# Optimization experiments

Measured on AMD Instinct MI355X. Metric: run time of the kernel, lower is better.

Reference implementation:

```python
import jax, jax.numpy as jnp
import numpy as np

B, N, X_DIM, Y_DIM, K = 256, 65536, 32, 64, 8
SIGMA_INIT = 0.01

def setup_inputs() -> dict:
    key = jax.random.key(0)
    k1, k2, k3, k4 = jax.random.split(key, 4)
    return {
        "x": jax.random.normal(k1, (B, X_DIM), dtype=jnp.float32),
        "pos_matrix": jax.random.normal(k2, (N, X_DIM), dtype=jnp.float32),
        "project_matrix": jax.random.normal(k3, (N, X_DIM, K), dtype=jnp.float32),
        "color_matrix": jax.random.normal(k4, (N, Y_DIM), dtype=jnp.float32),
        "sigma_matrix": jnp.full((N, K), SIGMA_INIT, dtype=jnp.float32),
    }

def reference(x, pos_matrix, project_matrix, color_matrix, sigma_matrix):
    # x_diff = (x[:,None,:] - pos[None,:,:]) @ P  -> (B, N, k)
    # computed without materializing (B, N, x_dim):
    xP = jnp.einsum('bi,nio->bno', x, project_matrix)          # (B, N, k)
    posP = jnp.einsum('ni,nio->no', pos_matrix, project_matrix)  # (N, k)
    x_diff = xP - posP[None, :, :]                               # (B, N, k)
    # Gaussian kernel per modality
    g = jnp.exp(-x_diff ** 2 / (2.0 * sigma_matrix ** 2))        # (B, N, k)
    # color = g^T @ color_matrix per batch -> (B, k, y_dim)
    color = jnp.einsum('bnk,ny->bky', g, color_matrix)
    return color
```

## Files before the change

kernel.cpp:

```cpp
#include <hip/hip_runtime.h>


typedef __attribute__((ext_vector_type(8))) short short8;
typedef __attribute__((ext_vector_type(4))) float f32x4;

#define NTOT   65536
#define XD     32
#define YD     64
#define KK     8
#define META_BYTES (NTOT*KK*8)
#define PART_FLOATS 32768
#define NCHUNKS 2048

__device__ __forceinline__ unsigned short f2bf(float f) {
  unsigned u = __float_as_uint(f);
  u += 0x7FFFu + ((u >> 16) & 1u);
  return (unsigned short)(u >> 16);
}

__device__ __forceinline__ void gload16(const void* g, void* l) {
  __builtin_amdgcn_global_load_lds(
      (const __attribute__((address_space(1))) unsigned*)g,
      (__attribute__((address_space(3))) unsigned*)l, 16, 0, 0);
}

union FragU { unsigned u[4]; short8 s8; };

__global__ __launch_bounds__(256)
void gaf_pre(const float* __restrict__ pos, const float* __restrict__ proj,
             const float* __restrict__ sig, float2* __restrict__ meta) {
  int gid = blockIdx.x * 256 + threadIdx.x;
  int n = gid >> 3, k = gid & 7;
  const float*  pk = proj + (size_t)n * XD * KK + k;
  const float4* pg = (const float4*)(pos + (size_t)n * XD);
  float d = 0.f;
#pragma unroll
  for (int j = 0; j < 8; ++j) {
    float4 v = pg[j];
    d = fmaf(v.x, pk[(4*j+0)*KK], d);
    d = fmaf(v.y, pk[(4*j+1)*KK], d);
    d = fmaf(v.z, pk[(4*j+2)*KK], d);
    d = fmaf(v.w, pk[(4*j+3)*KK], d);
  }
  float s = sig[gid];
  meta[gid] = make_float2(d, -0.72134752044448169f / (s * s));
}

__global__ __launch_bounds__(512, 4)
void gaf_main(const float* __restrict__ x, const float* __restrict__ proj,
              const float* __restrict__ colr, const float2* __restrict__ meta,
              float* __restrict__ partial, int NCH, int NR) {
  __shared__ unsigned short sPool[2*256*40 + 64*40];
  __shared__ float sPosP[8][36];
  __shared__ float sInv[8][36];
  __shared__ __align__(16) float rawP[32*XD*KK];
  unsigned short (*sPb0)[40] = (unsigned short(*)[40])sPool;
  unsigned short (*sPb1)[40] = (unsigned short(*)[40])(sPool + 256*40);
  unsigned short (*sCol)[40] = (unsigned short(*)[40])(sPool + 2*256*40);

  const int t = threadIdx.x, l = t & 63, w = t >> 6;

  int nr, sblk;
  {
    const int gid = blockIdx.x;
    if ((NR & 7) == 0) {
      const int xcd = gid & 7, j = gid >> 3;
      nr   = xcd * (NR >> 3) + (j >> 2);
      sblk = j & 3;
    } else { nr = gid >> 2; sblk = gid & 3; }
  }

  const int bt = w & 3, k0 = (w >> 2) * 4;
  const int lc = l & 15, lg = l >> 4;
  const int cbeg = nr * NCH;
  int cend = cbeg + NCH; if (cend > NCHUNKS) cend = NCHUNKS;

  float* pb = partial + (size_t)(nr * 4 + sblk) * PART_FLOATS;
  if (cbeg >= cend) {
    float4 z = {0.f,0.f,0.f,0.f};
#pragma unroll
    for (int r = 0; r < PART_FLOATS/4/512; ++r) ((float4*)pb)[t + r*512] = z;
    return;
  }

  short8 xf0, xf1;
  {
    const int brow = sblk*64 + bt*16 + lc;
    const float4* xr = (const float4*)(x + (size_t)brow*XD + lg*8);
    float4 u0 = xr[0], u1 = xr[1];
    float xv[8] = {u0.x,u0.y,u0.z,u0.w,u1.x,u1.y,u1.z,u1.w};
#pragma unroll
    for (int j = 0; j < 8; ++j) {
      unsigned u = __float_as_uint(xv[j]);
      unsigned short h0 = (unsigned short)(u >> 16);
      float r1 = xv[j] - __uint_as_float(u & 0xFFFF0000u);
      xf0[j] = (short)h0;
      xf1[j] = (short)f2bf(r1);
    }
  }

  f32x4 acc[4][4];
#pragma unroll
  for (int a = 0; a < 4; ++a)
#pragma unroll
    for (int b = 0; b < 4; ++b) acc[a][b] = (f32x4){0.f,0.f,0.f,0.f};

  const float4* colr4 = (const float4*)colr;

  auto ISSUE_P = [&](int c) {
    const float4* Pg = (const float4*)(proj + (size_t)c * 32 * XD * KK);
#pragma unroll
    for (int r = 0; r < 4; ++r)
      gload16(Pg + (t + r*512), &rawP[(w*64 + r*512) * 4]);
  };

  ISSUE_P(cbeg);
  for (int c = cbeg; c < cend; ++c) {
    __syncthreads();
    float4 cpf = colr4[(size_t)c * 512 + t];
    float2 mpf;
    if (t < 256) mpf = meta[(size_t)c * 256 + t];
    {
      const float4* raw4 = (const float4*)rawP;
#pragma unroll
      for (int r = 0; r < 2; ++r) {
        const int f0 = ((t >> 1) << 2) + (t & 1) + r * 1024;
        float4 va = raw4[f0], vb = raw4[f0 + 2];
        const int nn = (f0 >> 6) & 31, i0 = (f0 & 63) >> 1, kk4 = (f0 & 1) << 2;
        float ea[4] = {va.x, va.y, va.z, va.w};
        float eb[4] = {vb.x, vb.y, vb.z, vb.w};
#pragma unroll
        for (int jj = 0; jj < 4; ++jj) {
          const int row = (kk4 + jj) * 32 + nn;
          unsigned hi, lo;
          asm("v_cvt_pk_bf16_f32 %0, %1, %2" : "=v"(hi) : "v"(ea[jj]), "v"(eb[jj]));
          float r0 = ea[jj] - __uint_as_float(hi << 16);
          float r1 = eb[jj] - __uint_as_float(hi & 0xFFFF0000u);
          asm("v_cvt_pk_bf16_f32 %0, %1, %2" : "=v"(lo) : "v"(r0), "v"(r1));
          *(unsigned*)&sPb0[row][i0] = hi;
          *(unsigned*)&sPb1[row][i0] = lo;
        }
      }
    }
    {
      int n = t >> 4, y4 = (t & 15) * 4;
      sCol[y4+0][n] = f2bf(cpf.x);
      sCol[y4+1][n] = f2bf(cpf.y);
      sCol[y4+2][n] = f2bf(cpf.z);
      sCol[y4+3][n] = f2bf(cpf.w);
    }
    if (t < 256) { sPosP[t&7][t>>3] = mpf.x; sInv[t&7][t>>3] = mpf.y; }
    __syncthreads();
    if (c + 1 < cend) ISSUE_P(c + 1);

#pragma unroll
    for (int kk = 0; kk < 4; ++kk) {
      const int k = k0 + kk;
      FragU gb;
      {
        const int prow = k*32 + lc;
        short8 p0 = *(const short8*)&sPb0[prow][lg*8];
        short8 p1 = *(const short8*)&sPb1[prow][lg*8];
        f32x4 S = (f32x4){0.f,0.f,0.f,0.f};
        S = __builtin_amdgcn_mfma_f32_16x16x32_bf16(p1, xf1, S, 0, 0, 0);
        S = __builtin_amdgcn_mfma_f32_16x16x32_bf16(p1, xf0, S, 0, 0, 0);
        S = __builtin_amdgcn_mfma_f32_16x16x32_bf16(p0, xf1, S, 0, 0, 0);
        S = __builtin_amdgcn_mfma_f32_16x16x32_bf16(p0, xf0, S, 0, 0, 0);
        float4 pp = *(const float4*)&sPosP[k][lg*4];
        float4 iv = *(const float4*)&sInv[k][lg*4];
        float d0 = S[0]-pp.x, d1 = S[1]-pp.y, d2 = S[2]-pp.z, d3 = S[3]-pp.w;
        float g0 = __builtin_amdgcn_exp2f(d0*d0*iv.x);
        float g1 = __builtin_amdgcn_exp2f(d1*d1*iv.y);
        float g2 = __builtin_amdgcn_exp2f(d2*d2*iv.z);
        float g3 = __builtin_amdgcn_exp2f(d3*d3*iv.w);
        asm("v_cvt_pk_bf16_f32 %0, %1, %2" : "=v"(gb.u[0]) : "v"(g0), "v"(g1));
        asm("v_cvt_pk_bf16_f32 %0, %1, %2" : "=v"(gb.u[1]) : "v"(g2), "v"(g3));
      }
      {
        const int prow = k*32 + 16 + lc;
        short8 p0 = *(const short8*)&sPb0[prow][lg*8];
        short8 p1 = *(const short8*)&sPb1[prow][lg*8];
        f32x4 S = (f32x4){0.f,0.f,0.f,0.f};
        S = __builtin_amdgcn_mfma_f32_16x16x32_bf16(p1, xf1, S, 0, 0, 0);
        S = __builtin_amdgcn_mfma_f32_16x16x32_bf16(p1, xf0, S, 0, 0, 0);
        S = __builtin_amdgcn_mfma_f32_16x16x32_bf16(p0, xf1, S, 0, 0, 0);
        S = __builtin_amdgcn_mfma_f32_16x16x32_bf16(p0, xf0, S, 0, 0, 0);
        float4 pp = *(const float4*)&sPosP[k][16 + lg*4];
        float4 iv = *(const float4*)&sInv[k][16 + lg*4];
        float d0 = S[0]-pp.x, d1 = S[1]-pp.y, d2 = S[2]-pp.z, d3 = S[3]-pp.w;
        float g0 = __builtin_amdgcn_exp2f(d0*d0*iv.x);
        float g1 = __builtin_amdgcn_exp2f(d1*d1*iv.y);
        float g2 = __builtin_amdgcn_exp2f(d2*d2*iv.z);
        float g3 = __builtin_amdgcn_exp2f(d3*d3*iv.w);
        asm("v_cvt_pk_bf16_f32 %0, %1, %2" : "=v"(gb.u[2]) : "v"(g0), "v"(g1));
        asm("v_cvt_pk_bf16_f32 %0, %1, %2" : "=v"(gb.u[3]) : "v"(g2), "v"(g3));
      }
#pragma unroll
      for (int ys = 0; ys < 4; ++ys) {
        FragU af;
        *(uint2*)&af.u[0] = *(const uint2*)&sCol[ys*16 + lc][lg*4];
        *(uint2*)&af.u[2] = *(const uint2*)&sCol[ys*16 + lc][16 + lg*4];
        acc[kk][ys] = __builtin_amdgcn_mfma_f32_16x16x32_bf16(af.s8, gb.s8,
                                                              acc[kk][ys], 0, 0, 0);
      }
    }
  }
  __syncthreads();

  float* epi = (float*)sPool + w * (64*17);
#pragma unroll
  for (int kk = 0; kk < 4; ++kk) {
    const int k = k0 + kk;
#pragma unroll
    for (int ys = 0; ys < 4; ++ys) {
#pragma unroll
      for (int r = 0; r < 4; ++r)
        epi[(ys*16 + lg*4 + r)*17 + lc] = acc[kk][ys][r];
    }
    __syncthreads();
#pragma unroll
    for (int it = 0; it < 4; ++it) {
      int bi = it*4 + lg, y0 = lc*4;
      float4 v = { epi[(y0+0)*17 + bi], epi[(y0+1)*17 + bi],
                   epi[(y0+2)*17 + bi], epi[(y0+3)*17 + bi] };
      *(float4*)&pb[(size_t)(bt*16 + bi)*512 + k*64 + y0] = v;
    }
    __syncthreads();
  }
}

__global__ __launch_bounds__(512)
void gaf_reduce(const float* __restrict__ partial, float* __restrict__ out, int NR) {
  const int b = blockIdx.x;
  const int s = b >> 6, bl = b & 63;
  const int t = threadIdx.x;
  float a0 = 0.f, a1 = 0.f, a2 = 0.f, a3 = 0.f;
  int nr = 0;
  for (; nr + 4 <= NR; nr += 4) {
    a0 += partial[(size_t)((nr+0)*4 + s)*PART_FLOATS + bl*512 + t];
    a1 += partial[(size_t)((nr+1)*4 + s)*PART_FLOATS + bl*512 + t];
    a2 += partial[(size_t)((nr+2)*4 + s)*PART_FLOATS + bl*512 + t];
    a3 += partial[(size_t)((nr+3)*4 + s)*PART_FLOATS + bl*512 + t];
  }
  for (; nr < NR; ++nr)
    a0 += partial[(size_t)(nr*4 + s)*PART_FLOATS + bl*512 + t];
  out[(size_t)b*512 + t] = (a0 + a1) + (a2 + a3);
}

extern "C" void kernel_launch(void* const* d_in, const int* in_sizes, int n_in,
                              void* d_out, int out_size, void* d_ws, size_t ws_size,
                              hipStream_t stream) {
  const float* x    = (const float*)d_in[0];
  const float* pos  = (const float*)d_in[1];
  const float* proj = (const float*)d_in[2];
  const float* colr = (const float*)d_in[3];
  const float* sig  = (const float*)d_in[4];
  float* out = (float*)d_out;

  float2* meta    = (float2*)d_ws;
  float*  partial = (float*)((char*)d_ws + META_BYTES);

  size_t avail = (ws_size > META_BYTES) ? ws_size - META_BYTES : 0;
  int NR = (int)(avail / (4ull * PART_FLOATS * 4ull));
  if (NR > 128) NR = 128;
  if (NR < 1)  NR = 1;
  if (NR >= 8) NR &= ~7;
  int NCH = (NCHUNKS + NR - 1) / NR;

  gaf_pre<<<(NTOT*KK)/256, 256, 0, stream>>>(pos, proj, sig, meta);
  gaf_main<<<4*NR, 512, 0, stream>>>(x, proj, colr, meta, partial, NCH, NR);
  gaf_reduce<<<256, 512, 0, stream>>>(partial, out, NR);
}
```

Baseline: 105.8 us.

## Repack projection tiles into MFMA fragment order with padded staging to cut LDS conflicts

The raw projection staging buffer gets a padded per-row stride (260 floats), and the bf16 hi/lo projection tiles are stored directly in per-lane MFMA fragment order, so each lane reads its operand as one contiguous 16-byte load. The color tile load is reorganized so each thread gathers four n-values for one y and writes them as a packed uint2 using hardware bf16 conversion instead of four scalar software-rounded stores. The aim is fewer LDS bank conflicts and fewer LDS instructions in the per-chunk staging and the MFMA operand fetch. The price is more complex index math and strided global reads of the color matrix.

```diff
diff --git a/kernel.cpp b/kernel.cpp
--- a/kernel.cpp
+++ b/kernel.cpp
@@ -11,12 +11,7 @@
 #define META_BYTES (NTOT*KK*8)
 #define PART_FLOATS 32768
 #define NCHUNKS 2048
-
-__device__ __forceinline__ unsigned short f2bf(float f) {
-  unsigned u = __float_as_uint(f);
-  u += 0x7FFFu + ((u >> 16) & 1u);
-  return (unsigned short)(u >> 16);
-}
+#define CSTR   40
 
 __device__ __forceinline__ void gload16(const void* g, void* l) {
   __builtin_amdgcn_global_load_lds(
@@ -50,13 +45,13 @@
 void gaf_main(const float* __restrict__ x, const float* __restrict__ proj,
               const float* __restrict__ colr, const float2* __restrict__ meta,
               float* __restrict__ partial, int NCH, int NR) {
-  __shared__ unsigned short sPool[2*256*40 + 64*40];
+  __shared__ __align__(16) unsigned short sPool[16*512*2 + 64*CSTR];
   __shared__ float sPosP[8][36];
   __shared__ float sInv[8][36];
-  __shared__ __align__(16) float rawP[32*XD*KK];
-  unsigned short (*sPb0)[40] = (unsigned short(*)[40])sPool;
-  unsigned short (*sPb1)[40] = (unsigned short(*)[40])(sPool + 256*40);
-  unsigned short (*sCol)[40] = (unsigned short(*)[40])(sPool + 2*256*40);
+  __shared__ __align__(16) float rawP[32*260];
+  unsigned short* sPb0 = sPool;
+  unsigned short* sPb1 = sPool + 16*512;
+  unsigned short (*sCol)[CSTR] = (unsigned short(*)[CSTR])(sPool + 2*16*512);
 
   const int t = threadIdx.x, l = t & 63, w = t >> 6;
 
@@ -94,8 +89,10 @@
       unsigned u = __float_as_uint(xv[j]);
       unsigned short h0 = (unsigned short)(u >> 16);
       float r1 = xv[j] - __uint_as_float(u & 0xFFFF0000u);
+      unsigned ur = __float_as_uint(r1);
+      ur += 0x7FFFu + ((ur >> 16) & 1u);
       xf0[j] = (short)h0;
-      xf1[j] = (short)f2bf(r1);
+      xf1[j] = (short)(unsigned short)(ur >> 16);
     }
   }
 
@@ -105,49 +102,59 @@
 #pragma unroll
     for (int b = 0; b < 4; ++b) acc[a][b] = (f32x4){0.f,0.f,0.f,0.f};
 
-  const float4* colr4 = (const float4*)colr;
+  const int kp  = l & 1;
+  const int ipL = (l >> 1) & 3;
+  const int nS  = ((l >> 3) & 7) | ((w & 3) << 3);
+  const int sS  = nS >> 4;
+  const int ldst= (nS & 15);
 
   auto ISSUE_P = [&](int c) {
     const float4* Pg = (const float4*)(proj + (size_t)c * 32 * XD * KK);
 #pragma unroll
-    for (int r = 0; r < 4; ++r)
-      gload16(Pg + (t + r*512), &rawP[(w*64 + r*512) * 4]);
+    for (int r2 = 0; r2 < 4; ++r2) {
+      const int nd = w + r2*8;
+      gload16(Pg + nd*64 + l, &rawP[nd*260]);
+    }
   };
 
   ISSUE_P(cbeg);
   for (int c = cbeg; c < cend; ++c) {
     __syncthreads();
-    float4 cpf = colr4[(size_t)c * 512 + t];
+    const int yq = w*8 + (l>>3);
+    const int nq = (l&7)*4;
+    const float* cb = colr + (size_t)(c*32 + nq)*YD + yq;
+    float c0 = cb[0], c1 = cb[YD], c2 = cb[2*YD], c3 = cb[3*YD];
     float2 mpf;
     if (t < 256) mpf = meta[(size_t)c * 256 + t];
     {
       const float4* raw4 = (const float4*)rawP;
 #pragma unroll
       for (int r = 0; r < 2; ++r) {
-        const int f0 = ((t >> 1) << 2) + (t & 1) + r * 1024;
+        const int ip = ipL | (((w >> 2) & 1) << 2) | (r << 3);
+        const int f0 = nS * 65 + ip * 4 + kp;
         float4 va = raw4[f0], vb = raw4[f0 + 2];
-        const int nn = (f0 >> 6) & 31, i0 = (f0 & 63) >> 1, kk4 = (f0 & 1) << 2;
+        const int l_dst = ldst | ((ip >> 2) << 4);
+        const int wd = ip & 3;
         float ea[4] = {va.x, va.y, va.z, va.w};
         float eb[4] = {vb.x, vb.y, vb.z, vb.w};
 #pragma unroll
         for (int jj = 0; jj < 4; ++jj) {
-          const int row = (kk4 + jj) * 32 + nn;
+          const int ks = (kp*4 + jj)*2 + sS;
           unsigned hi, lo;
           asm("v_cvt_pk_bf16_f32 %0, %1, %2" : "=v"(hi) : "v"(ea[jj]), "v"(eb[jj]));
           float r0 = ea[jj] - __uint_as_float(hi << 16);
           float r1 = eb[jj] - __uint_as_float(hi & 0xFFFF0000u);
           asm("v_cvt_pk_bf16_f32 %0, %1, %2" : "=v"(lo) : "v"(r0), "v"(r1));
-          *(unsigned*)&sPb0[row][i0] = hi;
-          *(unsigned*)&sPb1[row][i0] = lo;
+          ((unsigned*)sPb0)[ks*256 + l_dst*4 + wd] = hi;
+          ((unsigned*)sPb1)[ks*256 + l_dst*4 + wd] = lo;
         }
       }
     }
     {
-      int n = t >> 4, y4 = (t & 15) * 4;
-      sCol[y4+0][n] = f2bf(cpf.x);
-      sCol[y4+1][n] = f2bf(cpf.y);
-      sCol[y4+2][n] = f2bf(cpf.z);
-      sCol[y4+3][n] = f2bf(cpf.w);
+      unsigned w0, w1;
+      asm("v_cvt_pk_bf16_f32 %0, %1, %2" : "=v"(w0) : "v"(c0), "v"(c1));
+      asm("v_cvt_pk_bf16_f32 %0, %1, %2" : "=v"(w1) : "v"(c2), "v"(c3));
+      *(uint2*)&sCol[yq][nq] = make_uint2(w0, w1);
     }
     if (t < 256) { sPosP[t&7][t>>3] = mpf.x; sInv[t&7][t>>3] = mpf.y; }
     __syncthreads();
@@ -158,9 +165,8 @@
       const int k = k0 + kk;
       FragU gb;
       {
-        const int prow = k*32 + lc;
-        short8 p0 = *(const short8*)&sPb0[prow][lg*8];
-        short8 p1 = *(const short8*)&sPb1[prow][lg*8];
+        short8 p0 = *(const short8*)&sPb0[(k*2+0)*512 + l*8];
+        short8 p1 = *(const short8*)&sPb1[(k*2+0)*512 + l*8];
         f32x4 S = (f32x4){0.f,0.f,0.f,0.f};
         S = __builtin_amdgcn_mfma_f32_16x16x32_bf16(p1, xf1, S, 0, 0, 0);
         S = __builtin_amdgcn_mfma_f32_16x16x32_bf16(p1, xf0, S, 0, 0, 0);
@@ -177,9 +183,8 @@
         asm("v_cvt_pk_bf16_f32 %0, %1, %2" : "=v"(gb.u[1]) : "v"(g2), "v"(g3));
       }
       {
-        const int prow = k*32 + 16 + lc;
-        short8 p0 = *(const short8*)&sPb0[prow][lg*8];
-        short8 p1 = *(const short8*)&sPb1[prow][lg*8];
+        short8 p0 = *(const short8*)&sPb0[(k*2+1)*512 + l*8];
+        short8 p1 = *(const short8*)&sPb1[(k*2+1)*512 + l*8];
         f32x4 S = (f32x4){0.f,0.f,0.f,0.f};
         S = __builtin_amdgcn_mfma_f32_16x16x32_bf16(p1, xf1, S, 0, 0, 0);
         S = __builtin_amdgcn_mfma_f32_16x16x32_bf16(p1, xf0, S, 0, 0, 0);
```

Measured after the change: 105.5 us, median of 2. Within noise of the previous version (-0.3%).
